# Optimization experiments

Measured on AMD Instinct MI355X. Metric: run time of the kernel, lower is better.

## Reference

```python
import jax, jax.numpy as jnp
import numpy as np

K = 512
U = 2
TEMP_BERN = 0.67
TEMP_CAT = 0.67
EULER = 0.5772156649015329
EPS = 1e-8
UEPS = 1e-6


def setup_inputs() -> dict:
    key = jax.random.key(0)
    ks = jax.random.split(key, 3)
    B, D = 16384, 1024
    inputs = jax.random.normal(ks[0], (B, D), jnp.float32)
    # glorot-normal-ish init for mW
    mW = jax.random.normal(ks[1], (D, K * U), jnp.float32) * jnp.sqrt(2.0 / (D + K * U))
    sW = jnp.full((D, K * U), -5.0, jnp.float32)
    conc1 = jnp.full((K,), 2.0, jnp.float32)
    conc0 = jnp.full((K,), 0.5453, jnp.float32)
    t_pi = jax.random.uniform(ks[2], (D, K), jnp.float32, 4.0, 5.0)
    biases = jnp.full((K * U,), 0.1, jnp.float32)
    return {"inputs": inputs, "mW": mW, "sW": sW, "conc1": conc1,
            "conc0": conc0, "t_pi": t_pi, "biases": biases}


def _uniform(k, shape):
    return jax.random.uniform(k, shape, jnp.float32, UEPS, 1.0 - UEPS)


def reference(inputs, mW, sW, conc1, conc0, t_pi, biases):
    rk = jax.random.split(jax.random.key(42), 4)

    # --- reparameterized weights W = mW + eps * softplus(sW) ---
    sW_sp = jax.nn.softplus(sW)
    eps = jax.lax.stop_gradient(jax.random.normal(rk[0], mW.shape, jnp.float32))
    W = mW + eps * sW_sp
    kl_weights = -0.5 * jnp.mean(2.0 * sW_sp - jnp.square(mW) - jnp.square(sW_sp) + 1.0)
    layer_loss = kl_weights / 60000.0

    # --- IBP: relaxed Bernoulli sample of t_pi ([D, K]) ---
    u = _uniform(rk[1], t_pi.shape)
    logistic = jnp.log(u) - jnp.log1p(-u)
    z_sample = jax.nn.sigmoid((t_pi + logistic) / TEMP_BERN)  # bin_concrete_sample
    z = jnp.tile(z_sample, (1, U))  # [D, K*U], column order u*K+k (as in TF code)

    # Kumaraswamy stick-breaking prior: cumprod along axis 0 (TF default)
    a_sp = jax.nn.softplus(conc1)  # [K]
    b_sp = jax.nn.softplus(conc0)  # [K]
    uk = _uniform(rk[2], t_pi.shape)
    q_u = jnp.power(1.0 - jnp.power(uk, 1.0 / b_sp), 1.0 / a_sp)  # kumaraswamy_sample
    prior_pi = jnp.cumprod(q_u, axis=0)
    q = jax.nn.sigmoid(t_pi)
    kl_z = jnp.sum(q * (jnp.log(q + EPS) - jnp.log(prior_pi + EPS)))

    # KL(Kumaraswamy(a,b) || Beta(1,1)); (beta-1) series term vanishes
    kl_sticks = jnp.sum(((a_sp - 1.0) / a_sp) * (-EULER - jax.scipy.special.digamma(b_sp) - 1.0 / b_sp)
                        + jnp.log(a_sp * b_sp + EPS) - (b_sp - 1.0) / b_sp)
    layer_loss = layer_loss + kl_sticks + kl_z

    W = z * W
    out = inputs @ W + biases  # [B, K*U]

    # --- LWTA activation via Gumbel-softmax over U competitors ---
    logits = out.reshape(-1, K, U)  # [B, K, U]
    g = -jnp.log(-jnp.log(_uniform(rk[3], logits.shape)))
    xi = jax.nn.softmax((logits + g) / TEMP_CAT, axis=-1)  # concrete_sample
    out_act = (logits * xi).reshape(out.shape)
    q_xi = jax.nn.softmax(logits, axis=-1)
    kl_xi = jnp.mean(jnp.sum(q_xi * (jnp.log(q_xi + EPS) - jnp.log(1.0 / U)), axis=1))
    layer_loss = layer_loss + kl_xi

    return out_act, layer_loss
```

## Files before the change

### kernel.cpp

```cpp
#include <hip/hip_runtime.h>
#include <stdint.h>
#include <math.h>

#define B_N   16384
#define D_N   1024
#define K_N   512
#define KU_N  1024
#define EPS_F 1e-8f
#define TEMP  0.67f
#define EULERC 0.5772156649015329f

#define HEPS  524288
#define HU    262144
#define HG    8388608

typedef uint32_t u32;
typedef __attribute__((ext_vector_type(4))) float f32x4;
typedef __attribute__((ext_vector_type(8))) __bf16 bf16x8;

#define TF_ROT(x, r) (((x) << (r)) | ((x) >> (32 - (r))))

__host__ __device__ static inline void threefry2x32(u32 k0, u32 k1,
                                                    u32 x0, u32 x1,
                                                    u32* o0, u32* o1) {
  u32 ks2 = k0 ^ k1 ^ 0x1BD11BDAu;
  x0 += k0; x1 += k1;
  x0 += x1; x1 = TF_ROT(x1, 13); x1 ^= x0;
  x0 += x1; x1 = TF_ROT(x1, 15); x1 ^= x0;
  x0 += x1; x1 = TF_ROT(x1, 26); x1 ^= x0;
  x0 += x1; x1 = TF_ROT(x1, 6);  x1 ^= x0;
  x0 += k1; x1 += ks2 + 1u;
  x0 += x1; x1 = TF_ROT(x1, 17); x1 ^= x0;
  x0 += x1; x1 = TF_ROT(x1, 29); x1 ^= x0;
  x0 += x1; x1 = TF_ROT(x1, 16); x1 ^= x0;
  x0 += x1; x1 = TF_ROT(x1, 24); x1 ^= x0;
  x0 += ks2; x1 += k0 + 2u;
  x0 += x1; x1 = TF_ROT(x1, 13); x1 ^= x0;
  x0 += x1; x1 = TF_ROT(x1, 15); x1 ^= x0;
  x0 += x1; x1 = TF_ROT(x1, 26); x1 ^= x0;
  x0 += x1; x1 = TF_ROT(x1, 6);  x1 ^= x0;
  x0 += k0; x1 += k1 + 3u;
  x0 += x1; x1 = TF_ROT(x1, 17); x1 ^= x0;
  x0 += x1; x1 = TF_ROT(x1, 29); x1 ^= x0;
  x0 += x1; x1 = TF_ROT(x1, 16); x1 ^= x0;
  x0 += x1; x1 = TF_ROT(x1, 24); x1 ^= x0;
  x0 += k1; x1 += ks2 + 4u;
  x0 += x1; x1 = TF_ROT(x1, 13); x1 ^= x0;
  x0 += x1; x1 = TF_ROT(x1, 15); x1 ^= x0;
  x0 += x1; x1 = TF_ROT(x1, 26); x1 ^= x0;
  x0 += x1; x1 = TF_ROT(x1, 6);  x1 ^= x0;
  x0 += ks2; x1 += k0 + 5u;
  *o0 = x0; *o1 = x1;
}

__device__ static inline float bits_to_u01(u32 b) {
  u32 f = (b >> 9) | 0x3f800000u;
  return __uint_as_float(f) - 1.0f;
}
__device__ static inline float unif_f(u32 b, float lo, float hi) {
  float f = bits_to_u01(b);
  return fmaxf(lo, f * (hi - lo) + lo);
}
__device__ static inline float erfinv_f(float x) {
  float w = -log1pf(-x * x);
  float p;
  if (w < 5.f) {
    w -= 2.5f;
    p = 2.81022636e-08f;
    p = fmaf(p, w, 3.43273939e-07f);
    p = fmaf(p, w, -3.5233877e-06f);
    p = fmaf(p, w, -4.39150654e-06f);
    p = fmaf(p, w, 0.00021858087f);
    p = fmaf(p, w, -0.00125372503f);
    p = fmaf(p, w, -0.00417768164f);
    p = fmaf(p, w, 0.246640727f);
    p = fmaf(p, w, 1.50140941f);
  } else {
    w = sqrtf(w) - 3.f;
    p = -0.000200214257f;
    p = fmaf(p, w, 0.000100950558f);
    p = fmaf(p, w, 0.00134934322f);
    p = fmaf(p, w, -0.00367342844f);
    p = fmaf(p, w, 0.00573950773f);
    p = fmaf(p, w, -0.0076224613f);
    p = fmaf(p, w, 0.00943887047f);
    p = fmaf(p, w, 1.00167406f);
    p = fmaf(p, w, 2.83297682f);
  }
  return p * x;
}
__device__ static inline float softplus_f(float x) {
  return fmaxf(x, 0.f) + log1pf(expf(-fabsf(x)));
}
__device__ static inline float rcp_f(float x) { return __builtin_amdgcn_rcpf(x); }
__device__ static inline float sigmoid_fast(float x) {
  return rcp_f(1.f + __expf(-x));
}
__device__ static inline float digamma_f(float x) {
  float r = 0.f;
  while (x < 6.f) { r -= 1.f / x; x += 1.f; }
  float inv = 1.f / x, inv2 = inv * inv;
  return r + logf(x) - 0.5f * inv
       - inv2 * (1.f / 12.f - inv2 * (1.f / 120.f - inv2 * (1.f / 252.f)));
}
__device__ static inline unsigned short f2bf_rne(float x) {
  u32 u = __float_as_uint(x);
  u32 r = (u + 0x7fffu + ((u >> 16) & 1u)) >> 16;
  return (unsigned short)r;
}
__device__ static inline u32 cvt_pk_bf16(float lo, float hi) {
  u32 r;
  asm("v_cvt_pk_bf16_f32 %0, %1, %2" : "=v"(r) : "v"(lo), "v"(hi));
  return r;
}
__device__ static inline void gload_lds16(const void* g, void* l) {
  __builtin_amdgcn_global_load_lds(
      (const __attribute__((address_space(1))) u32*)g,
      (__attribute__((address_space(3))) u32*)l, 16, 0, 0);
}

__device__ static inline float block_sum(float v) {
  __shared__ float sm[16];
  int lane = threadIdx.x & 63;
  int wid = threadIdx.x >> 6;
  #pragma unroll
  for (int o = 32; o > 0; o >>= 1) v += __shfl_down(v, o, 64);
  if (lane == 0) sm[wid] = v;
  __syncthreads();
  float s = 0.f;
  if (threadIdx.x == 0) {
    int nw = (blockDim.x + 63) >> 6;
    s = sm[0];
    for (int w = 1; w < nw; ++w) s += sm[w];
  }
  return s;
}

__global__ void k_init(const float* __restrict__ conc1,
                       const float* __restrict__ conc0,
                       float* __restrict__ invA, float* __restrict__ invB,
                       float* acc) {
  int k = threadIdx.x;
  float a = softplus_f(conc1[k]);
  float b = softplus_f(conc0[k]);
  invA[k] = 1.f / a;
  invB[k] = 1.f / b;
  float s = ((a - 1.f) / a) * (-EULERC - digamma_f(b) - 1.f / b)
          + logf(a * b + EPS_F) - (b - 1.f) / b;
  float t = block_sum(s);
  if (threadIdx.x == 0) { acc[0] = 0.f; acc[1] = t; }
}

__global__ __launch_bounds__(256) void k_qu(const float* __restrict__ invA,
                                            const float* __restrict__ invB,
                                            float* __restrict__ qu,
                                            u32 qk0, u32 qk1) {
  int i = blockIdx.x * 256 + threadIdx.x;
  u32 b0, b1;
  threefry2x32(qk0, qk1, (u32)i, (u32)(i + HU), &b0, &b1);
  const float lo = 1e-6f, hi = 1.f - 1e-6f;
  #pragma unroll
  for (int h = 0; h < 2; ++h) {
    int n = i + h * HU;
    u32 qb = h ? b1 : b0;
    int k = n & (K_N - 1);
    float u = unif_f(qb, lo, hi);
    qu[n] = powf(1.f - powf(u, invB[k]), invA[k]);
  }
}

__global__ __launch_bounds__(256) void k_klz_a(const float* __restrict__ qu,
                                               float* __restrict__ P) {
  int idx = blockIdx.x * 256 + threadIdx.x;
  int c = idx >> 9, k = idx & (K_N - 1);
  float p = 1.f;
  int d0 = c * 128;
  #pragma unroll 8
  for (int d = d0; d < d0 + 128; ++d) p *= qu[d * K_N + k];
  P[c * K_N + k] = p;
}

__global__ __launch_bounds__(256) void k_klz_b(const float* __restrict__ t_pi,
                                               const float* __restrict__ qu,
                                               const float* __restrict__ P,
                                               float* acc) {
  int idx = blockIdx.x * 256 + threadIdx.x;
  int c = idx >> 9, k = idx & (K_N - 1);
  float prior = 1.f;
  for (int c2 = 0; c2 < c; ++c2) prior *= P[c2 * K_N + k];
  float s = 0.f;
  int d0 = c * 128;
  #pragma unroll 4
  for (int d = d0; d < d0 + 128; ++d) {
    int n = d * K_N + k;
    prior *= qu[n];
    float q = sigmoid_fast(t_pi[n]);
    s += q * (__logf(q + EPS_F) - __logf(prior + EPS_F));
  }
  float t = block_sum(s);
  if (threadIdx.x == 0) atomicAdd(&acc[1], t);
}

__global__ __launch_bounds__(256) void k_wbuildT(const float* __restrict__ mW,
                                                 const float* __restrict__ sW,
                                                 const float* __restrict__ t_pi,
                                                 unsigned short* __restrict__ WzT,
                                                 float* acc,
                                                 u32 ek0, u32 ek1,
                                                 u32 uk0, u32 uk1) {
  int idx = blockIdx.x * 256 + threadIdx.x;
  int j = idx >> 9;
  int dlo = idx & 511;
  int kk = j & (K_N - 1);

  int n0 = dlo * KU_N + j;
  u32 e0, e1;
  threefry2x32(ek0, ek1, (u32)n0, (u32)(n0 + HEPS), &e0, &e1);
  int nz0 = dlo * K_N + kk;
  u32 z0b, z1b;
  threefry2x32(uk0, uk1, (u32)nz0, (u32)(nz0 + HU), &z0b, &z1b);

  const float lo = 1e-6f, hi = 1.f - 1e-6f;
  const float nlo = -0.99999994f, nhi = 1.0f;
  float klw = 0.f;
  {
    float u = unif_f(z0b, lo, hi);
    float logistic = __logf(u) - log1pf(-u);
    float z = sigmoid_fast((t_pi[nz0] + logistic) * (1.f / TEMP));
    float un = unif_f(e0, nlo, nhi);
    float epsn = 1.41421356f * erfinv_f(un);
    float m = mW[n0], sp = softplus_f(sW[n0]);
    float W = m + epsn * sp;
    WzT[j * D_N + dlo] = f2bf_rne(z * W);
    klw += 2.f * sp - m * m - sp * sp + 1.f;
  }
  {
    int n1 = n0 + HEPS;
    int nz1 = nz0 + HU;
    float u = unif_f(z1b, lo, hi);
    float logistic = __logf(u) - log1pf(-u);
    float z = sigmoid_fast((t_pi[nz1] + logistic) * (1.f / TEMP));
    float un = unif_f(e1, nlo, nhi);
    float epsn = 1.41421356f * erfinv_f(un);
    float m = mW[n1], sp = softplus_f(sW[n1]);
    float W = m + epsn * sp;
    WzT[j * D_N + dlo + 512] = f2bf_rne(z * W);
    klw += 2.f * sp - m * m - sp * sp + 1.f;
  }
  float t = block_sum(klw);
  if (threadIdx.x == 0) atomicAdd(&acc[0], t);
}

#define GBM 128
#define GBN 128
#define GBK 32

__global__ __launch_bounds__(256) void k_gemm(const float* __restrict__ A,
                                              const unsigned short* __restrict__ Bt,
                                              const float* __restrict__ bias,
                                              float* __restrict__ C) {
  __shared__ float As[GBM * GBK];
  __shared__ unsigned short Bs[GBN * GBK];

  const int tid = threadIdx.x;
  const int lane = tid & 63;
  const int w = tid >> 6;
  const int brow = blockIdx.y * GBM;
  const int bcol = blockIdx.x * GBN;

  const int arr = tid >> 3;
  const int aco = ((tid & 7) ^ (arr & 7)) << 2;
  const float* gA = A + (brow + arr) * D_N + aco;
  const int brr = tid >> 2;
  const int bco = ((tid & 3) ^ (brr & 3)) << 3;
  const unsigned short* gB = Bt + (bcol + brr) * D_N + bco;

  f32x4 acc[4][4];
  #pragma unroll
  for (int m = 0; m < 4; ++m)
    #pragma unroll
    for (int n = 0; n < 4; ++n) acc[m][n] = (f32x4){0.f, 0.f, 0.f, 0.f};

  const int wr = (w >> 1) << 6;
  const int wc = (w & 1) << 6;
  const int fr = lane & 15;
  const int kg = lane >> 4;

  union BF8 { u32 u[4]; bf16x8 v; };

  for (int kt = 0; kt < D_N; kt += GBK) {
    #pragma unroll
    for (int q = 0; q < 4; ++q)
      gload_lds16(gA + q * (32 * D_N) + kt, (char*)As + q * 4096 + (w << 10));
    #pragma unroll
    for (int q = 0; q < 2; ++q)
      gload_lds16(gB + q * (64 * D_N) + kt, (char*)Bs + q * 4096 + (w << 10));
    __syncthreads();

    BF8 af[4];
    #pragma unroll
    for (int m = 0; m < 4; ++m) {
      int row = wr + m * 16 + fr;
      int r7 = row & 7;
      const float* pa = As + row * GBK;
      f32x4 lov = *(const f32x4*)(pa + ((((kg << 1)    ) ^ r7) << 2));
      f32x4 hiv = *(const f32x4*)(pa + ((((kg << 1) | 1) ^ r7) << 2));
      af[m].u[0] = cvt_pk_bf16(lov.x, lov.y);
      af[m].u[1] = cvt_pk_bf16(lov.z, lov.w);
      af[m].u[2] = cvt_pk_bf16(hiv.x, hiv.y);
      af[m].u[3] = cvt_pk_bf16(hiv.z, hiv.w);
    }
    #pragma unroll
    for (int n = 0; n < 4; ++n) {
      int col = wc + n * 16 + fr;
      bf16x8 bf = *(const bf16x8*)(Bs + col * GBK + ((kg ^ (col & 3)) << 3));
      #pragma unroll
      for (int m = 0; m < 4; ++m)
        acc[m][n] = __builtin_amdgcn_mfma_f32_16x16x32_bf16(af[m].v, bf, acc[m][n], 0, 0, 0);
    }
    __syncthreads();
  }

  #pragma unroll
  for (int n = 0; n < 4; ++n) {
    int col = bcol + wc + n * 16 + fr;
    float bv = bias[col];
    #pragma unroll
    for (int m = 0; m < 4; ++m) {
      int rowb = brow + wr + m * 16 + (kg << 2);
      C[(rowb + 0) * KU_N + col] = acc[m][n].x + bv;
      C[(rowb + 1) * KU_N + col] = acc[m][n].y + bv;
      C[(rowb + 2) * KU_N + col] = acc[m][n].z + bv;
      C[(rowb + 3) * KU_N + col] = acc[m][n].w + bv;
    }
  }
}

__device__ static inline float lwta_row(float* C, int row, int k,
                                        u32 g0b, u32 g1b) {
  const float lo = 1e-6f, hi = 1.f - 1e-6f;
  int base = row * KU_N + (k << 1);
  float2 l = *(float2*)&C[base];
  float u0 = unif_f(g0b, lo, hi);
  float u1 = unif_f(g1b, lo, hi);
  float g0 = -__logf(-__logf(u0));
  float g1 = -__logf(-__logf(u1));
  const float it = 1.f / TEMP;
  float d = (l.y + g1) * it - (l.x + g0) * it;
  float xi0 = rcp_f(1.f + __expf(d));
  float xi1 = 1.f - xi0;
  float2 o;
  o.x = l.x * xi0;
  o.y = l.y * xi1;
  *(float2*)&C[base] = o;
  float qd = l.y - l.x;
  float q0 = rcp_f(1.f + __expf(qd));
  float q1 = 1.f - q0;
  const float LOG_HALF = -0.6931471805599453f;
  return q0 * (__logf(q0 + EPS_F) - LOG_HALF) + q1 * (__logf(q1 + EPS_F) - LOG_HALF);
}

__global__ __launch_bounds__(256) void k_epi(float* __restrict__ C,
                                             float* __restrict__ partial,
                                             u32 gk0, u32 gk1) {
  int idx = blockIdx.x * 256 + threadIdx.x;
  int b = idx >> 9;
  int k = idx & (K_N - 1);
  u32 m = ((u32)b << 10) + ((u32)k << 1);
  u32 p0a, p0b, p1a, p1b;
  threefry2x32(gk0, gk1, m, m + HG, &p0a, &p0b);
  threefry2x32(gk0, gk1, m + 1u, m + 1u + HG, &p1a, &p1b);
  float kl = lwta_row(C, b, k, p0a, p1a) + lwta_row(C, b + 8192, k, p0b, p1b);
  float t = block_sum(kl);
  if (threadIdx.x == 0) partial[blockIdx.x] = t;
}

__global__ void k_final(const float* __restrict__ acc,
                        const float* __restrict__ partial, int npart,
                        float* __restrict__ out_loss) {
  float s = 0.f;
  for (int i = threadIdx.x; i < npart; i += blockDim.x) s += partial[i];
  float t = block_sum(s);
  if (threadIdx.x == 0) {
    float kl_weights = -0.5f * (acc[0] / 1048576.f);
    out_loss[0] = kl_weights / 60000.f + acc[1] + t / 32768.f;
  }
}

extern "C" void kernel_launch(void* const* d_in, const int* in_sizes, int n_in,
                              void* d_out, int out_size, void* d_ws, size_t ws_size,
                              hipStream_t stream) {
  (void)in_sizes; (void)n_in; (void)out_size; (void)ws_size;
  const float* inputs = (const float*)d_in[0];
  const float* mW     = (const float*)d_in[1];
  const float* sW     = (const float*)d_in[2];
  const float* conc1  = (const float*)d_in[3];
  const float* conc0  = (const float*)d_in[4];
  const float* t_pi   = (const float*)d_in[5];
  const float* biases = (const float*)d_in[6];
  float* out = (float*)d_out;

  u32 a[4], b[4];
  for (int i = 0; i < 4; ++i)
    threefry2x32(0u, 42u, (u32)i, (u32)(i + 4), &a[i], &b[i]);
  u32 e_k0 = a[0], e_k1 = a[1];
  u32 u_k0 = a[2], u_k1 = a[3];
  u32 q_k0 = b[0], q_k1 = b[1];
  u32 g_k0 = b[2], g_k1 = b[3];

  char* wsb = (char*)d_ws;
  unsigned short* WzT = (unsigned short*)wsb;
  float* qu      = (float*)(wsb + (2u << 20));
  float* Pch     = (float*)(wsb + (4u << 20));
  float* invA    = (float*)(wsb + (4u << 20) + (16u << 10));
  float* invB    = (float*)(wsb + (4u << 20) + (18u << 10));
  float* acc     = (float*)(wsb + (4u << 20) + (20u << 10));
  float* partial = (float*)(wsb + (4u << 20) + (24u << 10));

  hipLaunchKernelGGL(k_init, dim3(1), dim3(512), 0, stream,
                     conc1, conc0, invA, invB, acc);
  hipLaunchKernelGGL(k_qu, dim3(HU / 256), dim3(256), 0, stream,
                     invA, invB, qu, q_k0, q_k1);
  hipLaunchKernelGGL(k_klz_a, dim3(16), dim3(256), 0, stream, qu, Pch);
  hipLaunchKernelGGL(k_klz_b, dim3(16), dim3(256), 0, stream,
                     t_pi, qu, Pch, acc);
  hipLaunchKernelGGL(k_wbuildT, dim3(HEPS / 256), dim3(256), 0, stream,
                     mW, sW, t_pi, WzT, acc, e_k0, e_k1, u_k0, u_k1);
  hipLaunchKernelGGL(k_gemm, dim3(KU_N / GBN, B_N / GBM), dim3(256), 0, stream,
                     inputs, WzT, biases, out);
  hipLaunchKernelGGL(k_epi, dim3(8192 * 512 / 256), dim3(256), 0, stream,
                     out, partial, g_k0, g_k1);
  hipLaunchKernelGGL(k_final, dim3(1), dim3(256), 0, stream,
                     acc, partial, 16384, out + 16777216);
}
```

Measured before the change: 213.2 us.

## Fuse LWTA epilogue into GEMM, recompute Kumaraswamy samples, tile weight transpose

Several changes at once. The Gumbel-softmax LWTA activation and its KL term now run in the GEMM epilogue, so C is no longer written and then re-read by a separate kernel. Each block pairs rows b and b+8192 so the threefry draws match the reference layout, and the partner logit comes from a lane shuffle. The q_u buffer is removed: its samples are regenerated inside the two KL-z kernels, which now run across more chunks. The weight build uses an LDS tile transpose for coalesced writes, and GEMM blocks are remapped in a grouped order for better L2 reuse. The risks are extra RNG arithmetic in the GEMM epilogue and more register pressure there.

```diff
diff --git a/kernel.cpp b/kernel.cpp
--- a/kernel.cpp
+++ b/kernel.cpp
@@ -139,7 +139,7 @@
 __global__ void k_init(const float* __restrict__ conc1,
                        const float* __restrict__ conc0,
                        float* __restrict__ invA, float* __restrict__ invB,
-                       float* acc) {
+                       float* gacc) {
   int k = threadIdx.x;
   float a = softplus_f(conc1[k]);
   float b = softplus_f(conc0[k]);
@@ -148,132 +148,138 @@
   float s = ((a - 1.f) / a) * (-EULERC - digamma_f(b) - 1.f / b)
           + logf(a * b + EPS_F) - (b - 1.f) / b;
   float t = block_sum(s);
-  if (threadIdx.x == 0) { acc[0] = 0.f; acc[1] = t; }
-}
-
-__global__ __launch_bounds__(256) void k_qu(const float* __restrict__ invA,
-                                            const float* __restrict__ invB,
-                                            float* __restrict__ qu,
-                                            u32 qk0, u32 qk1) {
-  int i = blockIdx.x * 256 + threadIdx.x;
-  u32 b0, b1;
-  threefry2x32(qk0, qk1, (u32)i, (u32)(i + HU), &b0, &b1);
-  const float lo = 1e-6f, hi = 1.f - 1e-6f;
-  #pragma unroll
-  for (int h = 0; h < 2; ++h) {
-    int n = i + h * HU;
-    u32 qb = h ? b1 : b0;
-    int k = n & (K_N - 1);
-    float u = unif_f(qb, lo, hi);
-    qu[n] = powf(1.f - powf(u, invB[k]), invA[k]);
-  }
-}
-
-__global__ __launch_bounds__(256) void k_klz_a(const float* __restrict__ qu,
-                                               float* __restrict__ P) {
+  if (threadIdx.x == 0) { gacc[0] = 0.f; gacc[1] = t; gacc[2] = 0.f; }
+}
+
+__global__ __launch_bounds__(256) void k_klz_a(const float* __restrict__ invA,
+                                               const float* __restrict__ invB,
+                                               float* __restrict__ P,
+                                               u32 qk0, u32 qk1) {
   int idx = blockIdx.x * 256 + threadIdx.x;
   int c = idx >> 9, k = idx & (K_N - 1);
+  float iA = invA[k], iB = invB[k];
   float p = 1.f;
-  int d0 = c * 128;
-  #pragma unroll 8
-  for (int d = d0; d < d0 + 128; ++d) p *= qu[d * K_N + k];
-  P[c * K_N + k] = p;
+  int d0 = c << 4;
+  for (int d = d0; d < d0 + 16; ++d) {
+    int n = (d << 9) + k;
+    u32 x0 = (n < HU) ? (u32)n : (u32)(n - HU);
+    u32 o0, o1;
+    threefry2x32(qk0, qk1, x0, x0 + HU, &o0, &o1);
+    u32 bits = (n < HU) ? o0 : o1;
+    float u = unif_f(bits, 1e-6f, 1.f - 1e-6f);
+    p *= powf(1.f - powf(u, iB), iA);
+  }
+  P[idx] = p;
 }
 
 __global__ __launch_bounds__(256) void k_klz_b(const float* __restrict__ t_pi,
-                                               const float* __restrict__ qu,
+                                               const float* __restrict__ invA,
+                                               const float* __restrict__ invB,
                                                const float* __restrict__ P,
-                                               float* acc) {
+                                               float* gacc,
+                                               u32 qk0, u32 qk1) {
   int idx = blockIdx.x * 256 + threadIdx.x;
   int c = idx >> 9, k = idx & (K_N - 1);
+  float iA = invA[k], iB = invB[k];
   float prior = 1.f;
-  for (int c2 = 0; c2 < c; ++c2) prior *= P[c2 * K_N + k];
+  for (int c2 = 0; c2 < c; ++c2) prior *= P[(c2 << 9) + k];
   float s = 0.f;
-  int d0 = c * 128;
-  #pragma unroll 4
-  for (int d = d0; d < d0 + 128; ++d) {
-    int n = d * K_N + k;
-    prior *= qu[n];
+  int d0 = c << 4;
+  for (int d = d0; d < d0 + 16; ++d) {
+    int n = (d << 9) + k;
+    u32 x0 = (n < HU) ? (u32)n : (u32)(n - HU);
+    u32 o0, o1;
+    threefry2x32(qk0, qk1, x0, x0 + HU, &o0, &o1);
+    u32 bits = (n < HU) ? o0 : o1;
+    float u = unif_f(bits, 1e-6f, 1.f - 1e-6f);
+    prior *= powf(1.f - powf(u, iB), iA);
     float q = sigmoid_fast(t_pi[n]);
     s += q * (__logf(q + EPS_F) - __logf(prior + EPS_F));
   }
   float t = block_sum(s);
-  if (threadIdx.x == 0) atomicAdd(&acc[1], t);
+  if (threadIdx.x == 0) atomicAdd(&gacc[1], t);
 }
 
 __global__ __launch_bounds__(256) void k_wbuildT(const float* __restrict__ mW,
                                                  const float* __restrict__ sW,
                                                  const float* __restrict__ t_pi,
                                                  unsigned short* __restrict__ WzT,
-                                                 float* acc,
+                                                 float* __restrict__ gacc,
                                                  u32 ek0, u32 ek1,
                                                  u32 uk0, u32 uk1) {
-  int idx = blockIdx.x * 256 + threadIdx.x;
-  int j = idx >> 9;
-  int dlo = idx & 511;
+  __shared__ unsigned short tile[64][65];
+  int dt = (int)blockIdx.x >> 4;
+  int jt = (int)blockIdx.x & 15;
+  int d0 = dt << 6, j0 = jt << 6;
+  int tj = threadIdx.x & 63;
+  int tr = threadIdx.x >> 6;
+  int j = j0 + tj;
   int kk = j & (K_N - 1);
-
-  int n0 = dlo * KU_N + j;
-  u32 e0, e1;
-  threefry2x32(ek0, ek1, (u32)n0, (u32)(n0 + HEPS), &e0, &e1);
-  int nz0 = dlo * K_N + kk;
-  u32 z0b, z1b;
-  threefry2x32(uk0, uk1, (u32)nz0, (u32)(nz0 + HU), &z0b, &z1b);
-
-  const float lo = 1e-6f, hi = 1.f - 1e-6f;
-  const float nlo = -0.99999994f, nhi = 1.0f;
+  bool lowD = (dt < 8);
   float klw = 0.f;
-  {
-    float u = unif_f(z0b, lo, hi);
+  #pragma unroll 4
+  for (int rr = 0; rr < 16; ++rr) {
+    int dl = (rr << 2) + tr;
+    int d = d0 + dl;
+    int n = (d << 10) + j;
+    u32 x0 = lowD ? (u32)n : (u32)(n - HEPS);
+    u32 o0, o1;
+    threefry2x32(ek0, ek1, x0, x0 + HEPS, &o0, &o1);
+    u32 ebits = lowD ? o0 : o1;
+    int nz = (d << 9) + kk;
+    u32 zx0 = lowD ? (u32)nz : (u32)(nz - HU);
+    u32 z0, z1;
+    threefry2x32(uk0, uk1, zx0, zx0 + HU, &z0, &z1);
+    u32 zbits = lowD ? z0 : z1;
+    float u = unif_f(zbits, 1e-6f, 1.f - 1e-6f);
     float logistic = __logf(u) - log1pf(-u);
-    float z = sigmoid_fast((t_pi[nz0] + logistic) * (1.f / TEMP));
-    float un = unif_f(e0, nlo, nhi);
+    float z = sigmoid_fast((t_pi[nz] + logistic) * (1.f / TEMP));
+    float un = unif_f(ebits, -0.99999994f, 1.0f);
     float epsn = 1.41421356f * erfinv_f(un);
-    float m = mW[n0], sp = softplus_f(sW[n0]);
-    float W = m + epsn * sp;
-    WzT[j * D_N + dlo] = f2bf_rne(z * W);
+    float m = mW[n], sp = softplus_f(sW[n]);
+    tile[tj][dl] = f2bf_rne(z * (m + epsn * sp));
     klw += 2.f * sp - m * m - sp * sp + 1.f;
   }
-  {
-    int n1 = n0 + HEPS;
-    int nz1 = nz0 + HU;
-    float u = unif_f(z1b, lo, hi);
-    float logistic = __logf(u) - log1pf(-u);
-    float z = sigmoid_fast((t_pi[nz1] + logistic) * (1.f / TEMP));
-    float un = unif_f(e1, nlo, nhi);
-    float epsn = 1.41421356f * erfinv_f(un);
-    float m = mW[n1], sp = softplus_f(sW[n1]);
-    float W = m + epsn * sp;
-    WzT[j * D_N + dlo + 512] = f2bf_rne(z * W);
-    klw += 2.f * sp - m * m - sp * sp + 1.f;
+  __syncthreads();
+  #pragma unroll 4
+  for (int rr = 0; rr < 16; ++rr) {
+    int jl = (rr << 2) + tr;
+    WzT[(size_t)(j0 + jl) * D_N + d0 + tj] = tile[jl][tj];
   }
   float t = block_sum(klw);
-  if (threadIdx.x == 0) atomicAdd(&acc[0], t);
-}
-
-#define GBM 128
+  if (threadIdx.x == 0) atomicAdd(&gacc[0], t);
+}
+
 #define GBN 128
 #define GBK 32
 
 __global__ __launch_bounds__(256) void k_gemm(const float* __restrict__ A,
                                               const unsigned short* __restrict__ Bt,
                                               const float* __restrict__ bias,
-                                              float* __restrict__ C) {
-  __shared__ float As[GBM * GBK];
+                                              float* __restrict__ C,
+                                              float* __restrict__ gacc,
+                                              u32 gk0, u32 gk1) {
+  __shared__ float As[128 * GBK];
   __shared__ unsigned short Bs[GBN * GBK];
+
+  int f = (int)blockIdx.x;
+  int wk = (f & 7) * 128 + (f >> 3);
+  int by = wk >> 3;
+  int bxN = wk & 7;
+  const int brow = by * 64;
+  const int bcol = bxN * GBN;
 
   const int tid = threadIdx.x;
   const int lane = tid & 63;
   const int w = tid >> 6;
-  const int brow = blockIdx.y * GBM;
-  const int bcol = blockIdx.x * GBN;
 
   const int arr = tid >> 3;
   const int aco = ((tid & 7) ^ (arr & 7)) << 2;
-  const float* gA = A + (brow + arr) * D_N + aco;
+  const float* gA0 = A + (size_t)(brow + arr) * D_N + aco;
+  const float* gA1 = A + (size_t)(8192 + brow + arr) * D_N + aco;
   const int brr = tid >> 2;
   const int bco = ((tid & 3) ^ (brr & 3)) << 3;
-  const unsigned short* gB = Bt + (bcol + brr) * D_N + bco;
+  const unsigned short* gB = Bt + (size_t)(bcol + brr) * D_N + bco;
 
   f32x4 acc[4][4];
   #pragma unroll
@@ -281,7 +287,7 @@
     #pragma unroll
     for (int n = 0; n < 4; ++n) acc[m][n] = (f32x4){0.f, 0.f, 0.f, 0.f};
 
-  const int wr = (w >> 1) << 6;
+  const int wr2 = (w >> 1) << 5;
   const int wc = (w & 1) << 6;
   const int fr = lane & 15;
   const int kg = lane >> 4;
@@ -289,20 +295,20 @@
   union BF8 { u32 u[4]; bf16x8 v; };
 
   for (int kt = 0; kt < D_N; kt += GBK) {
-    #pragma unroll
-    for (int q = 0; q < 4; ++q)
-      gload_lds16(gA + q * (32 * D_N) + kt, (char*)As + q * 4096 + (w << 10));
-    #pragma unroll
-    for (int q = 0; q < 2; ++q)
-      gload_lds16(gB + q * (64 * D_N) + kt, (char*)Bs + q * 4096 + (w << 10));
+    gload_lds16(gA0 + kt,            (char*)As + 0 * 4096 + (w << 10));
+    gload_lds16(gA0 + 32 * D_N + kt, (char*)As + 1 * 4096 + (w << 10));
+    gload_lds16(gA1 + kt,            (char*)As + 2 * 4096 + (w << 10));
+    gload_lds16(gA1 + 32 * D_N + kt, (char*)As + 3 * 4096 + (w << 10));
+    gload_lds16(gB + kt,             (char*)Bs + 0 * 4096 + (w << 10));
+    gload_lds16(gB + 64 * D_N + kt,  (char*)Bs + 1 * 4096 + (w << 10));
     __syncthreads();
 
     BF8 af[4];
     #pragma unroll
     for (int m = 0; m < 4; ++m) {
-      int row = wr + m * 16 + fr;
-      int r7 = row & 7;
-      const float* pa = As + row * GBK;
+      int lr = (m < 2 ? wr2 + m * 16 : 64 + wr2 + (m - 2) * 16) + fr;
+      int r7 = lr & 7;
+      const float* pa = As + lr * GBK;
       f32x4 lov = *(const f32x4*)(pa + ((((kg << 1)    ) ^ r7) << 2));
       f32x4 hiv = *(const f32x4*)(pa + ((((kg << 1) | 1) ^ r7) << 2));
       af[m].u[0] = cvt_pk_bf16(lov.x, lov.y);
@@ -312,8 +318,8 @@
     }
     #pragma unroll
     for (int n = 0; n < 4; ++n) {
-      int col = wc + n * 16 + fr;
-      bf16x8 bf = *(const bf16x8*)(Bs + col * GBK + ((kg ^ (col & 3)) << 3));
+      int colL = wc + n * 16 + fr;
+      bf16x8 bf = *(const bf16x8*)(Bs + colL * GBK + ((kg ^ (colL & 3)) << 3));
       #pragma unroll
       for (int m = 0; m < 4; ++m)
         acc[m][n] = __builtin_amdgcn_mfma_f32_16x16x32_bf16(af[m].v, bf, acc[m][n], 0, 0, 0);
@@ -321,69 +327,54 @@
     __syncthreads();
   }
 
+  const float invT = 1.f / TEMP;
+  const float LOG2F = 0.6931471805599453f;
+  float klsum = 0.f;
   #pragma unroll
   for (int n = 0; n < 4; ++n) {
     int col = bcol + wc + n * 16 + fr;
     float bv = bias[col];
     #pragma unroll
-    for (int m = 0; m < 4; ++m) {
-      int rowb = brow + wr + m * 16 + (kg << 2);
-      C[(rowb + 0) * KU_N + col] = acc[m][n].x + bv;
-      C[(rowb + 1) * KU_N + col] = acc[m][n].y + bv;
-      C[(rowb + 2) * KU_N + col] = acc[m][n].z + bv;
-      C[(rowb + 3) * KU_N + col] = acc[m][n].w + bv;
+    for (int m = 0; m < 2; ++m) {
+      int r0 = brow + wr2 + m * 16 + (kg << 2);
+      #pragma unroll
+      for (int j = 0; j < 4; ++j) {
+        float v0 = acc[m][n][j] + bv;
+        float v1 = acc[m + 2][n][j] + bv;
+        int r = r0 + j;
+        u32 midx = (u32)(r * KU_N + col);
+        u32 b0, b1;
+        threefry2x32(gk0, gk1, midx, midx + HG, &b0, &b1);
+        float u0 = unif_f(b0, 1e-6f, 1.f - 1e-6f);
+        float u1 = unif_f(b1, 1e-6f, 1.f - 1e-6f);
+        float g0 = -__logf(-__logf(u0));
+        float g1 = -__logf(-__logf(u1));
+        float s0 = (v0 + g0) * invT;
+        float s1 = (v1 + g1) * invT;
+        float s0o = __shfl_xor(s0, 1, 64);
+        float s1o = __shfl_xor(s1, 1, 64);
+        float l0o = __shfl_xor(v0, 1, 64);
+        float l1o = __shfl_xor(v1, 1, 64);
+        float xi0 = rcp_f(1.f + __expf(s0o - s0));
+        float xi1 = rcp_f(1.f + __expf(s1o - s1));
+        C[(size_t)r * KU_N + col] = v0 * xi0;
+        C[(size_t)(r + 8192) * KU_N + col] = v1 * xi1;
+        float q0 = rcp_f(1.f + __expf(l0o - v0));
+        float q1 = rcp_f(1.f + __expf(l1o - v1));
+        klsum += q0 * (__logf(q0 + EPS_F) + LOG2F)
+               + q1 * (__logf(q1 + EPS_F) + LOG2F);
+      }
     }
   }
-}
-
-__device__ static inline float lwta_row(float* C, int row, int k,
-                                        u32 g0b, u32 g1b) {
-  const float lo = 1e-6f, hi = 1.f - 1e-6f;
-  int base = row * KU_N + (k << 1);
-  float2 l = *(float2*)&C[base];
-  float u0 = unif_f(g0b, lo, hi);
-  float u1 = unif_f(g1b, lo, hi);
-  float g0 = -__logf(-__logf(u0));
-  float g1 = -__logf(-__logf(u1));
-  const float it = 1.f / TEMP;
-  float d = (l.y + g1) * it - (l.x + g0) * it;
-  float xi0 = rcp_f(1.f + __expf(d));
-  float xi1 = 1.f - xi0;
-  float2 o;
-  o.x = l.x * xi0;
-  o.y = l.y * xi1;
-  *(float2*)&C[base] = o;
-  float qd = l.y - l.x;
-  float q0 = rcp_f(1.f + __expf(qd));
-  float q1 = 1.f - q0;
-  const float LOG_HALF = -0.6931471805599453f;
-  return q0 * (__logf(q0 + EPS_F) - LOG_HALF) + q1 * (__logf(q1 + EPS_F) - LOG_HALF);
-}
-
-__global__ __launch_bounds__(256) void k_epi(float* __restrict__ C,
-                                             float* __restrict__ partial,
-                                             u32 gk0, u32 gk1) {
-  int idx = blockIdx.x * 256 + threadIdx.x;
-  int b = idx >> 9;
-  int k = idx & (K_N - 1);
-  u32 m = ((u32)b << 10) + ((u32)k << 1);
-  u32 p0a, p0b, p1a, p1b;
-  threefry2x32(gk0, gk1, m, m + HG, &p0a, &p0b);
-  threefry2x32(gk0, gk1, m + 1u, m + 1u + HG, &p1a, &p1b);
-  float kl = lwta_row(C, b, k, p0a, p1a) + lwta_row(C, b + 8192, k, p0b, p1b);
-  float t = block_sum(kl);
-  if (threadIdx.x == 0) partial[blockIdx.x] = t;
-}
-
-__global__ void k_final(const float* __restrict__ acc,
-                        const float* __restrict__ partial, int npart,
+  float t = block_sum(klsum);
+  if (threadIdx.x == 0) atomicAdd(&gacc[2], t);
+}
+
+__global__ void k_final(const float* __restrict__ gacc,
                         float* __restrict__ out_loss) {
-  float s = 0.f;
-  for (int i = threadIdx.x; i < npart; i += blockDim.x) s += partial[i];
-  float t = block_sum(s);
   if (threadIdx.x == 0) {
-    float kl_weights = -0.5f * (acc[0] / 1048576.f);
-    out_loss[0] = kl_weights / 60000.f + acc[1] + t / 32768.f;
+    float kl_weights = -0.5f * (gacc[0] * (1.f / 1048576.f));
+    out_loss[0] = kl_weights / 60000.f + gacc[1] + gacc[2] * (1.f / 16384.f);
   }
 }
 
@@ -410,26 +401,21 @@
 
   char* wsb = (char*)d_ws;
   unsigned short* WzT = (unsigned short*)wsb;
-  float* qu      = (float*)(wsb + (2u << 20));
-  float* Pch     = (float*)(wsb + (4u << 20));
-  float* invA    = (float*)(wsb + (4u << 20) + (16u << 10));
-  float* invB    = (float*)(wsb + (4u << 20) + (18u << 10));
-  float* acc     = (float*)(wsb + (4u << 20) + (20u << 10));
-  float* partial = (float*)(wsb + (4u << 20) + (24u << 10));
+  float* P    = (float*)(wsb + (2u << 20));
+  float* invA = (float*)(wsb + (2u << 20) + (128u << 10));
+  float* invB = (float*)(wsb + (2u << 20) + (130u << 10));
+  float* gacc = (float*)(wsb + (2u << 20) + (132u << 10));
 
   hipLaunchKernelGGL(k_init, dim3(1), dim3(512), 0, stream,
-                     conc1, conc0, invA, invB, acc);
-  hipLaunchKernelGGL(k_qu, dim3(HU / 256), dim3(256), 0, stream,
-                     invA, invB, qu, q_k0, q_k1);
-  hipLaunchKernelGGL(k_klz_a, dim3(16), dim3(256), 0, stream, qu, Pch);
-  hipLaunchKernelGGL(k_klz_b, dim3(16), dim3(256), 0, stream,
-                     t_pi, qu, Pch, acc);
-  hipLaunchKernelGGL(k_wbuildT, dim3(HEPS / 256), dim3(256), 0, stream,
-                     mW, sW, t_pi, WzT, acc, e_k0, e_k1, u_k0, u_k1);
-  hipLaunchKernelGGL(k_gemm, dim3(KU_N / GBN, B_N / GBM), dim3(256), 0, stream,
-                     inputs, WzT, biases, out);
-  hipLaunchKernelGGL(k_epi, dim3(8192 * 512 / 256), dim3(256), 0, stream,
-                     out, partial, g_k0, g_k1);
-  hipLaunchKernelGGL(k_final, dim3(1), dim3(256), 0, stream,
-                     acc, partial, 16384, out + 16777216);
-}
+                     conc1, conc0, invA, invB, gacc);
+  hipLaunchKernelGGL(k_klz_a, dim3(128), dim3(256), 0, stream,
+                     invA, invB, P, q_k0, q_k1);
+  hipLaunchKernelGGL(k_klz_b, dim3(128), dim3(256), 0, stream,
+                     t_pi, invA, invB, P, gacc, q_k0, q_k1);
+  hipLaunchKernelGGL(k_wbuildT, dim3(256), dim3(256), 0, stream,
+                     mW, sW, t_pi, WzT, gacc, e_k0, e_k1, u_k0, u_k1);
+  hipLaunchKernelGGL(k_gemm, dim3(1024), dim3(256), 0, stream,
+                     inputs, WzT, biases, out, gacc, g_k0, g_k1);
+  hipLaunchKernelGGL(k_final, dim3(1), dim3(64), 0, stream,
+                     gacc, out + 16777216);
+}
```

After: 181.5 us. -14.9%, faster.
